# Performance work log

Measured on AMD Instinct MI355X. Metric: run time of the kernel, lower is better.

Reference implementation:

```python
import jax, jax.numpy as jnp
import numpy as np

NUM_CQ = 16
NUM_CODES = 8192
NUM_SAMPLES = 16
TEMP = 1.0
NHEADS = 4
DM = 32
EMB = 768
B, L = 64, 512


def setup_inputs():
    key = jax.random.key(0)
    ks = jax.random.split(key, 16)

    def lin(k, shape):
        fan_in = shape[-1]
        return (jax.random.uniform(k, shape, jnp.float32, -1.0, 1.0) / np.sqrt(fan_in)).astype(jnp.float32)

    xcq = jax.random.normal(ks[0], (B, L, EMB), jnp.float32)
    attn_mask = jax.random.randint(ks[1], (B, L - NUM_CQ), 0, 2, dtype=jnp.int32)
    cb = jax.random.normal(ks[2], (NUM_CODES, EMB), jnp.float32)
    codebook = 100.0 * cb / jnp.linalg.norm(cb, axis=-1, keepdims=True)  # matches 100*normalize init
    return dict(
        xcq=xcq, attn_mask=attn_mask,
        fc_in_w=lin(ks[3], (DM, EMB)), fc_in_b=jnp.zeros((DM,), jnp.float32),
        fc_out_w=lin(ks[4], (EMB, DM)), fc_out_b=jnp.zeros((EMB,), jnp.float32),
        enc_in_w=lin(ks[5], (2, 3 * DM, DM)), enc_in_b=jnp.zeros((2, 3 * DM), jnp.float32),
        enc_out_w=lin(ks[6], (2, DM, DM)), enc_out_b=jnp.zeros((2, DM), jnp.float32),
        enc_ff1_w=lin(ks[7], (2, 2 * DM, DM)), enc_ff1_b=jnp.zeros((2, 2 * DM), jnp.float32),
        enc_ff2_w=lin(ks[8], (2, DM, 2 * DM)), enc_ff2_b=jnp.zeros((2, DM), jnp.float32),
        enc_ln1_g=jnp.ones((2, DM), jnp.float32), enc_ln1_b=jnp.zeros((2, DM), jnp.float32),
        enc_ln2_g=jnp.ones((2, DM), jnp.float32), enc_ln2_b=jnp.zeros((2, DM), jnp.float32),
        codebook=codebook,
    )


def _layernorm(x, g, b):
    mu = jnp.mean(x, -1, keepdims=True)
    var = jnp.mean((x - mu) ** 2, -1, keepdims=True)
    return g * (x - mu) / jnp.sqrt(var + 1e-5) + b


def _forward(xcq, attn_mask, fc_in_w, fc_in_b, fc_out_w, fc_out_b,
             enc_in_w, enc_in_b, enc_out_w, enc_out_b,
             enc_ff1_w, enc_ff1_b, enc_ff2_w, enc_ff2_b,
             enc_ln1_g, enc_ln1_b, enc_ln2_g, enc_ln2_b, codebook):
    Bb, Ll, _ = xcq.shape
    dh = DM // NHEADS
    x = xcq @ fc_in_w.T + fc_in_b  # [B, L, 32]
    # ones for the cq tokens, then the provided mask; True = valid key
    valid = jnp.concatenate([jnp.ones((Bb, NUM_CQ), bool), attn_mask.astype(bool)], axis=1)  # [B, L]
    for l in range(2):  # torch post-norm TransformerEncoderLayer, relu, dropout=0 (eval)
        qkv = x @ enc_in_w[l].T + enc_in_b[l]
        q, k, v = jnp.split(qkv, 3, axis=-1)
        sh = lambda t: t.reshape(Bb, Ll, NHEADS, dh).transpose(0, 2, 1, 3)  # [B,h,L,dh]
        q, k, v = sh(q), sh(k), sh(v)
        scores = jnp.einsum('bhqd,bhkd->bhqk', q, k) / np.sqrt(dh)
        scores = jnp.where(valid[:, None, None, :], scores, -1e9)  # key padding mask
        attn = jax.nn.softmax(scores, axis=-1)
        o = jnp.einsum('bhqk,bhkd->bhqd', attn, v).transpose(0, 2, 1, 3).reshape(Bb, Ll, DM)
        o = o @ enc_out_w[l].T + enc_out_b[l]
        x = _layernorm(x + o, enc_ln1_g[l], enc_ln1_b[l])
        h = jax.nn.relu(x @ enc_ff1_w[l].T + enc_ff1_b[l]) @ enc_ff2_w[l].T + enc_ff2_b[l]
        x = _layernorm(x + h, enc_ln2_g[l], enc_ln2_b[l])
    xc_out = x[:, :NUM_CQ] @ fc_out_w.T + fc_out_b  # [B, ncq, 768]
    flat = xc_out.reshape(-1, EMB)  # [N, 768]
    dists = (jnp.sum(flat ** 2, 1, keepdims=True) + jnp.sum(codebook ** 2, 1)
             - 2.0 * (flat @ codebook.T))  # [N, K] squared euclidean
    logits = (-dists - 1e-5) / TEMP
    N = Bb * NUM_CQ
    # multinomial(total_count=NUM_SAMPLES): draw S categoricals per row and count
    draws = jax.random.categorical(jax.random.key(42), logits, shape=(NUM_SAMPLES, N))  # [S, N]
    rows = jnp.broadcast_to(jnp.arange(N), (NUM_SAMPLES, N))
    samples = jnp.zeros((N, NUM_CODES), jnp.float32).at[rows, draws].add(1.0)  # [N, K] counts
    xq = (samples @ codebook).reshape(xc_out.shape) / NUM_SAMPLES
    xc_quantized = xc_out + jax.lax.stop_gradient(xq - xc_out)  # straight-through estimator
    return xc_quantized


def reference(xcq, attn_mask, fc_in_w, fc_in_b, fc_out_w, fc_out_b,
              enc_in_w, enc_in_b, enc_out_w, enc_out_b,
              enc_ff1_w, enc_ff1_b, enc_ff2_w, enc_ff2_b,
              enc_ln1_g, enc_ln1_b, enc_ln2_g, enc_ln2_b, codebook):
    xc_quantized = _forward(xcq, attn_mask, fc_in_w, fc_in_b, fc_out_w, fc_out_b,
                            enc_in_w, enc_in_b, enc_out_w, enc_out_b,
                            enc_ff1_w, enc_ff1_b, enc_ff2_w, enc_ff2_b,
                            enc_ln1_g, enc_ln1_b, enc_ln2_g, enc_ln2_b, codebook)
    return (xc_quantized, xcq)
```

## Files before the change

kernel.cpp:

```cpp
#include <hip/hip_runtime.h>
#include <stdint.h>

#define NCODES 8192
#define NROWS 1024

#define OFF_LOGITS 0ll
#define OFF_X      8388608ll
#define OFF_QKV    9437184ll
#define OFF_ATTN   12582912ll
#define OFF_FLAT   13631488ll
#define OFF_CSQ    14418944ll

__device__ __forceinline__ uint32_t rotl32(uint32_t x, int r) { return (x << r) | (x >> (32 - r)); }

__device__ __forceinline__ void tf2x32_key42(uint32_t x0, uint32_t x1, uint32_t& o0, uint32_t& o1) {
  const uint32_t k0 = 0u, k1 = 42u;
  const uint32_t k2 = k0 ^ k1 ^ 0x1BD11BDAu;
  x0 += k0; x1 += k1;
  x0 += x1; x1 = rotl32(x1,13); x1 ^= x0;
  x0 += x1; x1 = rotl32(x1,15); x1 ^= x0;
  x0 += x1; x1 = rotl32(x1,26); x1 ^= x0;
  x0 += x1; x1 = rotl32(x1, 6); x1 ^= x0;
  x0 += k1; x1 += k2 + 1u;
  x0 += x1; x1 = rotl32(x1,17); x1 ^= x0;
  x0 += x1; x1 = rotl32(x1,29); x1 ^= x0;
  x0 += x1; x1 = rotl32(x1,16); x1 ^= x0;
  x0 += x1; x1 = rotl32(x1,24); x1 ^= x0;
  x0 += k2; x1 += k0 + 2u;
  x0 += x1; x1 = rotl32(x1,13); x1 ^= x0;
  x0 += x1; x1 = rotl32(x1,15); x1 ^= x0;
  x0 += x1; x1 = rotl32(x1,26); x1 ^= x0;
  x0 += x1; x1 = rotl32(x1, 6); x1 ^= x0;
  x0 += k0; x1 += k1 + 3u;
  x0 += x1; x1 = rotl32(x1,17); x1 ^= x0;
  x0 += x1; x1 = rotl32(x1,29); x1 ^= x0;
  x0 += x1; x1 = rotl32(x1,16); x1 ^= x0;
  x0 += x1; x1 = rotl32(x1,24); x1 ^= x0;
  x0 += k1; x1 += k2 + 4u;
  x0 += x1; x1 = rotl32(x1,13); x1 ^= x0;
  x0 += x1; x1 = rotl32(x1,15); x1 ^= x0;
  x0 += x1; x1 = rotl32(x1,26); x1 ^= x0;
  x0 += x1; x1 = rotl32(x1, 6); x1 ^= x0;
  x0 += k2; x1 += k0 + 5u;
  o0 = x0; o1 = x1;
}

__device__ __forceinline__ float gumbel_at(uint32_t idx) {
  uint32_t y0, y1;
  tf2x32_key42(0u, idx, y0, y1);
  uint32_t bits = y0 ^ y1;
  float f = __uint_as_float((bits >> 9) | 0x3f800000u) - 1.0f;
  float u = fmaxf(f, 1.17549435e-38f);
  return -logf(-logf(u));
}

__global__ __launch_bounds__(256) void k_fcin(const float* __restrict__ xcq,
                                              const float* __restrict__ W,
                                              const float* __restrict__ b,
                                              float* __restrict__ x,
                                              float* __restrict__ outcopy) {
  __shared__ float xs[64 * 36];
  int t = threadIdx.x;
  int w = t >> 6, lane = t & 63;
  long tb = (long)blockIdx.x * 64;
  const float4* xcq4 = (const float4*)xcq;
  float4* out4 = (float4*)outcopy;
  const float4* W4 = (const float4*)W;
  float acc[8];
  #pragma unroll
  for (int i = 0; i < 8; i++) acc[i] = 0.f;

  for (int jc4 = 0; jc4 < 192; jc4 += 8) {
    __syncthreads();
    #pragma unroll
    for (int p = 0; p < 2; p++) {
      int f = t + 256 * p;
      int row = f >> 3, j4 = f & 7;
      long g = (tb + row) * 192 + jc4 + j4;
      float4 v = xcq4[g];
      *(float4*)(xs + row * 36 + j4 * 4) = v;
      out4[g] = v;
    }
    __syncthreads();
    #pragma unroll
    for (int j4 = 0; j4 < 8; j4++) {
      float4 xv = *(const float4*)(xs + lane * 36 + j4 * 4);
      #pragma unroll
      for (int ci = 0; ci < 8; ci++) {
        int c = w * 8 + ci;
        float4 wv = W4[c * 192 + jc4 + j4];
        acc[ci] += xv.x * wv.x + xv.y * wv.y + xv.z * wv.z + xv.w * wv.w;
      }
    }
  }
  __syncthreads();
  *(float4*)(xs + lane * 36 + w * 8)     = make_float4(acc[0] + b[w*8+0], acc[1] + b[w*8+1], acc[2] + b[w*8+2], acc[3] + b[w*8+3]);
  *(float4*)(xs + lane * 36 + w * 8 + 4) = make_float4(acc[4] + b[w*8+4], acc[5] + b[w*8+5], acc[6] + b[w*8+6], acc[7] + b[w*8+7]);
  __syncthreads();
  float4* x4 = (float4*)x;
  #pragma unroll
  for (int p = 0; p < 2; p++) {
    int f = t + 256 * p;
    int row = f >> 3, c4 = f & 7;
    x4[(tb + row) * 8 + c4] = *(const float4*)(xs + row * 36 + c4 * 4);
  }
}

__global__ __launch_bounds__(64) void k_qkv(const float* __restrict__ x,
                                            const float* __restrict__ W,
                                            const float* __restrict__ b,
                                            float* __restrict__ qkv) {
  long token = (long)blockIdx.x * 64 + threadIdx.x;
  const float4* x4 = (const float4*)x;
  const float4* W4 = (const float4*)W;
  float4* q4 = (float4*)qkv;
  float4 xr[8];
  #pragma unroll
  for (int j4 = 0; j4 < 8; j4++) xr[j4] = x4[token * 8 + j4];
  #pragma unroll
  for (int c4 = 0; c4 < 24; c4++) {
    float s[4];
    #pragma unroll
    for (int q = 0; q < 4; q++) {
      int c = c4 * 4 + q;
      float acc = 0.f;
      #pragma unroll
      for (int j4 = 0; j4 < 8; j4++) {
        float4 wv = W4[c * 8 + j4];
        acc += xr[j4].x * wv.x + xr[j4].y * wv.y + xr[j4].z * wv.z + xr[j4].w * wv.w;
      }
      s[q] = acc + b[c];
    }
    q4[token * 24 + c4] = make_float4(s[0], s[1], s[2], s[3]);
  }
}

__global__ __launch_bounds__(256) void k_attn(const float* __restrict__ qkv,
                                              const int* __restrict__ amask,
                                              float* __restrict__ attno) {
  int z = blockIdx.x;
  int b = z >> 3;
  int h = (z >> 1) & 3;
  int half = z & 1;
  __shared__ float4 ks4[512 * 2];
  __shared__ float4 vs4[512 * 2];
  __shared__ float inval[512];
  int t = threadIdx.x;
  long qb4 = (long)b * 512 * 24;
  const float4* qkv4 = (const float4*)qkv;
  #pragma unroll
  for (int p = 0; p < 4; p++) {
    int f = t + 256 * p;
    int tok = f >> 1, hf = f & 1;
    ks4[f] = qkv4[qb4 + (long)tok * 24 + 8 + h * 2 + hf];
    vs4[f] = qkv4[qb4 + (long)tok * 24 + 16 + h * 2 + hf];
  }
  #pragma unroll
  for (int p = 0; p < 2; p++) {
    int l = t + 256 * p;
    inval[l] = (l < 16 || amask[b * 496 + (l - 16)] != 0) ? 0.f : 1.f;
  }
  __syncthreads();
  const float scale = 0.35355339059327373f;
  int lq = half * 256 + t;
  float4 qa = qkv4[qb4 + (long)lq * 24 + h * 2];
  float4 qb = qkv4[qb4 + (long)lq * 24 + h * 2 + 1];
  float m = -3.4e38f;
  for (int lk = 0; lk < 512; lk++) {
    float4 ka = ks4[lk * 2], kb = ks4[lk * 2 + 1];
    float s = qa.x*ka.x + qa.y*ka.y + qa.z*ka.z + qa.w*ka.w
            + qb.x*kb.x + qb.y*kb.y + qb.z*kb.z + qb.w*kb.w;
    s *= scale;
    s = inval[lk] != 0.f ? -1e9f : s;
    m = fmaxf(m, s);
  }
  float denom = 0.f;
  float4 o0 = make_float4(0,0,0,0), o1 = make_float4(0,0,0,0);
  for (int lk = 0; lk < 512; lk++) {
    float4 ka = ks4[lk * 2], kb = ks4[lk * 2 + 1];
    float s = qa.x*ka.x + qa.y*ka.y + qa.z*ka.z + qa.w*ka.w
            + qb.x*kb.x + qb.y*kb.y + qb.z*kb.z + qb.w*kb.w;
    s *= scale;
    s = inval[lk] != 0.f ? -1e9f : s;
    float p = expf(s - m);
    denom += p;
    float4 va = vs4[lk * 2], vb = vs4[lk * 2 + 1];
    o0.x += p * va.x; o0.y += p * va.y; o0.z += p * va.z; o0.w += p * va.w;
    o1.x += p * vb.x; o1.y += p * vb.y; o1.z += p * vb.z; o1.w += p * vb.w;
  }
  float inv = 1.f / denom;
  float4* a4 = (float4*)attno;
  long ob = ((long)b * 512 + lq) * 8 + h * 2;
  a4[ob]     = make_float4(o0.x*inv, o0.y*inv, o0.z*inv, o0.w*inv);
  a4[ob + 1] = make_float4(o1.x*inv, o1.y*inv, o1.z*inv, o1.w*inv);
}

__global__ __launch_bounds__(64) void k_oproj_ln(const float* __restrict__ attno,
                                                 const float* __restrict__ W,
                                                 const float* __restrict__ b,
                                                 const float* __restrict__ g,
                                                 const float* __restrict__ beta,
                                                 float* __restrict__ x) {
  long token = (long)blockIdx.x * 64 + threadIdx.x;
  const float4* a4 = (const float4*)attno;
  const float4* x4 = (const float4*)x;
  const float4* W4 = (const float4*)W;
  float4 orow[8];
  float xr[32];
  #pragma unroll
  for (int j4 = 0; j4 < 8; j4++) {
    orow[j4] = a4[token * 8 + j4];
    float4 v = x4[token * 8 + j4];
    xr[j4*4] = v.x; xr[j4*4+1] = v.y; xr[j4*4+2] = v.z; xr[j4*4+3] = v.w;
  }
  float v[32];
  #pragma unroll
  for (int c = 0; c < 32; c++) {
    float acc = 0.f;
    #pragma unroll
    for (int j4 = 0; j4 < 8; j4++) {
      float4 wv = W4[c * 8 + j4];
      acc += orow[j4].x * wv.x + orow[j4].y * wv.y + orow[j4].z * wv.z + orow[j4].w * wv.w;
    }
    v[c] = acc + b[c] + xr[c];
  }
  float mu = 0.f;
  #pragma unroll
  for (int c = 0; c < 32; c++) mu += v[c];
  mu *= 0.03125f;
  float var = 0.f;
  #pragma unroll
  for (int c = 0; c < 32; c++) { float d = v[c] - mu; var += d * d; }
  var *= 0.03125f;
  float inv = 1.f / sqrtf(var + 1e-5f);
  float4* xo4 = (float4*)x;
  #pragma unroll
  for (int j4 = 0; j4 < 8; j4++) {
    float4 o;
    o.x = g[j4*4]   * (v[j4*4]   - mu) * inv + beta[j4*4];
    o.y = g[j4*4+1] * (v[j4*4+1] - mu) * inv + beta[j4*4+1];
    o.z = g[j4*4+2] * (v[j4*4+2] - mu) * inv + beta[j4*4+2];
    o.w = g[j4*4+3] * (v[j4*4+3] - mu) * inv + beta[j4*4+3];
    xo4[token * 8 + j4] = o;
  }
}

__global__ __launch_bounds__(64) void k_ffn_ln(const float* __restrict__ x,
                                               const float* __restrict__ W1,
                                               const float* __restrict__ b1,
                                               const float* __restrict__ W2,
                                               const float* __restrict__ b2,
                                               const float* __restrict__ g,
                                               const float* __restrict__ beta,
                                               float* __restrict__ xout) {
  long token = (long)blockIdx.x * 64 + threadIdx.x;
  const float4* x4 = (const float4*)x;
  const float4* W14 = (const float4*)W1;
  const float4* W24 = (const float4*)W2;
  float xr[32];
  #pragma unroll
  for (int j4 = 0; j4 < 8; j4++) {
    float4 v = x4[token * 8 + j4];
    xr[j4*4] = v.x; xr[j4*4+1] = v.y; xr[j4*4+2] = v.z; xr[j4*4+3] = v.w;
  }
  float h[64];
  #pragma unroll
  for (int c = 0; c < 64; c++) {
    float acc = 0.f;
    #pragma unroll
    for (int j4 = 0; j4 < 8; j4++) {
      float4 wv = W14[c * 8 + j4];
      acc += xr[j4*4] * wv.x + xr[j4*4+1] * wv.y + xr[j4*4+2] * wv.z + xr[j4*4+3] * wv.w;
    }
    h[c] = fmaxf(acc + b1[c], 0.f);
  }
  float v[32];
  #pragma unroll
  for (int c = 0; c < 32; c++) {
    float acc = 0.f;
    #pragma unroll
    for (int j4 = 0; j4 < 16; j4++) {
      float4 wv = W24[c * 16 + j4];
      acc += h[j4*4] * wv.x + h[j4*4+1] * wv.y + h[j4*4+2] * wv.z + h[j4*4+3] * wv.w;
    }
    v[c] = acc + b2[c] + xr[c];
  }
  float mu = 0.f;
  #pragma unroll
  for (int c = 0; c < 32; c++) mu += v[c];
  mu *= 0.03125f;
  float var = 0.f;
  #pragma unroll
  for (int c = 0; c < 32; c++) { float d = v[c] - mu; var += d * d; }
  var *= 0.03125f;
  float inv = 1.f / sqrtf(var + 1e-5f);
  float4* xo4 = (float4*)xout;
  #pragma unroll
  for (int j4 = 0; j4 < 8; j4++) {
    float4 o;
    o.x = g[j4*4]   * (v[j4*4]   - mu) * inv + beta[j4*4];
    o.y = g[j4*4+1] * (v[j4*4+1] - mu) * inv + beta[j4*4+1];
    o.z = g[j4*4+2] * (v[j4*4+2] - mu) * inv + beta[j4*4+2];
    o.w = g[j4*4+3] * (v[j4*4+3] - mu) * inv + beta[j4*4+3];
    xo4[token * 8 + j4] = o;
  }
}

__global__ __launch_bounds__(256) void k_fcout(const float* __restrict__ x,
                                               const float* __restrict__ W,
                                               const float* __restrict__ b,
                                               float* __restrict__ flat) {
  int bb = blockIdx.x;
  __shared__ float xs[16 * 32];
  int t = threadIdx.x;
  if (t < 128) {
    int row = t >> 3, j4 = t & 7;
    *(float4*)(xs + row * 32 + j4 * 4) =
        *(const float4*)(x + ((long)bb * 512 + row) * 32 + j4 * 4);
  }
  __syncthreads();
  #pragma unroll
  for (int i = 0; i < 3; i++) {
    int e = t + 256 * i;
    const float4* w4 = (const float4*)(W + e * 32);
    float4 wv[8];
    #pragma unroll
    for (int j4 = 0; j4 < 8; j4++) wv[j4] = w4[j4];
    float bias = b[e];
    #pragma unroll
    for (int r = 0; r < 16; r++) {
      float s = 0.f;
      #pragma unroll
      for (int j4 = 0; j4 < 8; j4++) {
        const float* xr = xs + r * 32 + j4 * 4;
        s += xr[0] * wv[j4].x + xr[1] * wv[j4].y + xr[2] * wv[j4].z + xr[3] * wv[j4].w;
      }
      flat[((long)bb * 16 + r) * 768 + e] = s + bias;
    }
  }
}

__global__ __launch_bounds__(256) void k_cbsq(const float* __restrict__ cb,
                                              float* __restrict__ cb_sq) {
  int w = threadIdx.x >> 6, lane = threadIdx.x & 63;
  int k = blockIdx.x * 4 + w;
  const float* row = cb + (long)k * 768;
  float s = 0.f;
  #pragma unroll
  for (int i = 0; i < 12; i++) { float v = row[lane + 64 * i]; s += v * v; }
  #pragma unroll
  for (int off = 32; off >= 1; off >>= 1) s += __shfl_xor(s, off);
  if (lane == 0) cb_sq[k] = s;
}

__global__ __launch_bounds__(256, 2) void k_logits(const float* __restrict__ flat,
                                                   const float* __restrict__ cb,
                                                   const float* __restrict__ cb_sq,
                                                   float* __restrict__ logits) {
  int rb = blockIdx.x >> 5;
  int cblk = blockIdx.x & 31;
  __shared__ float fs[64 * 36];
  __shared__ float cs[256 * 36];
  int t = threadIdx.x;
  int r0 = (t >> 5) * 8;
  int c0 = t & 31;
  long frow = (long)rb * 64;
  long cbase = (long)cblk * 256;
  float acc[8][8];
  #pragma unroll
  for (int ri = 0; ri < 8; ri++)
    #pragma unroll
    for (int ci = 0; ci < 8; ci++) acc[ri][ci] = 0.f;

  for (int kc = 0; kc < 768; kc += 32) {
    __syncthreads();
    #pragma unroll
    for (int p = 0; p < 2; p++) {
      int f = t + 256 * p;
      int row = f >> 3, k4 = f & 7;
      *(float4*)(fs + row * 36 + k4 * 4) =
          *(const float4*)(flat + (frow + row) * 768 + kc + k4 * 4);
    }
    #pragma unroll
    for (int p = 0; p < 8; p++) {
      int col = p * 32 + (t >> 3), k4 = t & 7;
      *(float4*)(cs + col * 36 + k4 * 4) =
          *(const float4*)(cb + (cbase + col) * 768 + kc + k4 * 4);
    }
    __syncthreads();
    #pragma unroll
    for (int k4 = 0; k4 < 8; k4++) {
      float4 fa[8], fb[8];
      #pragma unroll
      for (int i = 0; i < 8; i++) fa[i] = *(const float4*)(fs + (r0 + i) * 36 + k4 * 4);
      #pragma unroll
      for (int i = 0; i < 8; i++) fb[i] = *(const float4*)(cs + (c0 + 32 * i) * 36 + k4 * 4);
      #pragma unroll
      for (int ri = 0; ri < 8; ri++) {
        #pragma unroll
        for (int ci = 0; ci < 8; ci++) {
          acc[ri][ci] = fmaf(fa[ri].x, fb[ci].x, acc[ri][ci]);
          acc[ri][ci] = fmaf(fa[ri].y, fb[ci].y, acc[ri][ci]);
          acc[ri][ci] = fmaf(fa[ri].z, fb[ci].z, acc[ri][ci]);
          acc[ri][ci] = fmaf(fa[ri].w, fb[ci].w, acc[ri][ci]);
        }
      }
    }
  }
  #pragma unroll
  for (int ci = 0; ci < 8; ci++) {
    long col = cbase + c0 + 32 * ci;
    float csq = cb_sq[col];
    #pragma unroll
    for (int ri = 0; ri < 8; ri++) {
      long n = frow + r0 + ri;
      logits[n * 8192 + col] = 2.f * acc[ri][ci] - csq - 1e-5f;
    }
  }
}

__global__ __launch_bounds__(256) void k_sample(const float* __restrict__ logits,
                                                const float* __restrict__ cb,
                                                const float* __restrict__ flat,
                                                float* __restrict__ out0) {
  int n = blockIdx.x, t = threadIdx.x;
  const float* lrow = logits + (long)n * 8192;
  __shared__ float s_max[4];
  __shared__ int s_cnt;
  __shared__ int cand[8192];
  __shared__ float redv[64];
  __shared__ int redi[64];
  __shared__ int draws[16];
  float m = -3.4e38f;
  for (int i = 0; i < 32; i++) m = fmaxf(m, lrow[t + 256 * i]);
  #pragma unroll
  for (int off = 32; off >= 1; off >>= 1) m = fmaxf(m, __shfl_xor(m, off));
  if ((t & 63) == 0) s_max[t >> 6] = m;
  if (t == 0) s_cnt = 0;
  __syncthreads();
  float rowmax = fmaxf(fmaxf(s_max[0], s_max[1]), fmaxf(s_max[2], s_max[3]));
  float thresh = rowmax - 20.5f;
  for (int i = 0; i < 32; i++) {
    int k = t + 256 * i;
    if (lrow[k] >= thresh) { int p = atomicAdd(&s_cnt, 1); cand[p] = k; }
  }
  __syncthreads();
  int ncand = s_cnt;
  float bv[16]; int bi[16];
  #pragma unroll
  for (int s = 0; s < 16; s++) { bv[s] = -3.4e38f; bi[s] = 0x7fffffff; }
  for (int c = t; c < ncand; c += 256) {
    int k = cand[c];
    float lg = lrow[k];
    #pragma unroll
    for (int s = 0; s < 16; s++) {
      uint32_t idx = ((uint32_t)((s << 10) + n) << 13) | (uint32_t)k;
      float val = gumbel_at(idx) + lg;
      if (val > bv[s] || (val == bv[s] && k < bi[s])) { bv[s] = val; bi[s] = k; }
    }
  }
  #pragma unroll
  for (int s = 0; s < 16; s++) {
    #pragma unroll
    for (int off = 32; off >= 1; off >>= 1) {
      float ov = __shfl_xor(bv[s], off);
      int oi = __shfl_xor(bi[s], off);
      if (ov > bv[s] || (ov == bv[s] && oi < bi[s])) { bv[s] = ov; bi[s] = oi; }
    }
    if ((t & 63) == 0) { redv[s * 4 + (t >> 6)] = bv[s]; redi[s * 4 + (t >> 6)] = bi[s]; }
  }
  __syncthreads();
  if (t < 16) {
    float bvv = redv[t * 4]; int bii = redi[t * 4];
    #pragma unroll
    for (int w = 1; w < 4; w++) {
      float ov = redv[t * 4 + w]; int oi = redi[t * 4 + w];
      if (ov > bvv || (ov == bvv && oi < bii)) { bvv = ov; bii = oi; }
    }
    draws[t] = bii;
  }
  __syncthreads();
  #pragma unroll
  for (int i = 0; i < 3; i++) {
    int e = t + 256 * i;
    float ssum = 0.f;
    #pragma unroll
    for (int s = 0; s < 16; s++) ssum += cb[(long)draws[s] * 768 + e];
    float xq = ssum * 0.0625f;
    float fl = flat[(long)n * 768 + e];
    out0[(long)n * 768 + e] = fl + (xq - fl);
  }
}

extern "C" void kernel_launch(void* const* d_in, const int* in_sizes, int n_in,
                              void* d_out, int out_size, void* d_ws, size_t ws_size,
                              hipStream_t stream) {
  (void)in_sizes; (void)n_in; (void)out_size; (void)ws_size;
  const float* xcq      = (const float*)d_in[0];
  const int*   amask    = (const int*)d_in[1];
  const float* fc_in_w  = (const float*)d_in[2];
  const float* fc_in_b  = (const float*)d_in[3];
  const float* fc_out_w = (const float*)d_in[4];
  const float* fc_out_b = (const float*)d_in[5];
  const float* enc_in_w = (const float*)d_in[6];
  const float* enc_in_b = (const float*)d_in[7];
  const float* enc_out_w= (const float*)d_in[8];
  const float* enc_out_b= (const float*)d_in[9];
  const float* ff1w     = (const float*)d_in[10];
  const float* ff1b     = (const float*)d_in[11];
  const float* ff2w     = (const float*)d_in[12];
  const float* ff2b     = (const float*)d_in[13];
  const float* ln1g     = (const float*)d_in[14];
  const float* ln1b     = (const float*)d_in[15];
  const float* ln2g     = (const float*)d_in[16];
  const float* ln2b     = (const float*)d_in[17];
  const float* cb       = (const float*)d_in[18];
  float* out = (float*)d_out;
  float* ws  = (float*)d_ws;

  float* x      = ws + OFF_X;
  float* qkv    = ws + OFF_QKV;
  float* attno  = ws + OFF_ATTN;
  float* flat   = ws + OFF_FLAT;
  float* csq    = ws + OFF_CSQ;
  float* logits = ws + OFF_LOGITS;

  k_fcin<<<512, 256, 0, stream>>>(xcq, fc_in_w, fc_in_b, x, out + 786432);
  for (int l = 0; l < 2; l++) {
    k_qkv<<<512, 64, 0, stream>>>(x, enc_in_w + l * 96 * 32, enc_in_b + l * 96, qkv);
    k_attn<<<512, 256, 0, stream>>>(qkv, amask, attno);
    k_oproj_ln<<<512, 64, 0, stream>>>(attno, enc_out_w + l * 32 * 32, enc_out_b + l * 32,
                                       ln1g + l * 32, ln1b + l * 32, x);
    k_ffn_ln<<<512, 64, 0, stream>>>(x, ff1w + l * 64 * 32, ff1b + l * 64,
                                     ff2w + l * 32 * 64, ff2b + l * 32,
                                     ln2g + l * 32, ln2b + l * 32, x);
  }
  k_fcout<<<64, 256, 0, stream>>>(x, fc_out_w, fc_out_b, flat);
  k_cbsq<<<2048, 256, 0, stream>>>(cb, csq);
  k_logits<<<512, 256, 0, stream>>>(flat, cb, csq, logits);
  k_sample<<<1024, 256, 0, stream>>>(logits, cb, flat, out);
}
```

Baseline: 1.108 ms.

## Compute approximate logits with bf16 MFMA and rescore candidates exactly in fp32

Replaces the fp32 SIMT logits GEMM with a bf16 MFMA GEMM on 128x128 tiles, with swizzled LDS so reads avoid bank conflicts. It first converts the codebook and the features to bf16 in separate kernels. Because bf16 scores are approximate, the sampler keeps a wider candidate window (rowmax-30 instead of -20.5) and recomputes exact fp32 dot products for those candidates before the Gumbel argmax. This trades the large fp32 GEMM for cheap matrix-core math, but adds conversion passes and per-candidate 768-length dot products, and relies on the widened threshold to preserve exact sampling.

```diff
diff --git a/kernel.cpp b/kernel.cpp
--- a/kernel.cpp
+++ b/kernel.cpp
@@ -353,96 +353,126 @@
   if (lane == 0) cb_sq[k] = s;
 }
 
-__global__ __launch_bounds__(256, 2) void k_logits(const float* __restrict__ flat,
-                                                   const float* __restrict__ cb,
-                                                   const float* __restrict__ cb_sq,
-                                                   float* __restrict__ logits) {
-  int rb = blockIdx.x >> 5;
-  int cblk = blockIdx.x & 31;
-  __shared__ float fs[64 * 36];
-  __shared__ float cs[256 * 36];
+__device__ __forceinline__ ushort f2bf(float x) {
+  uint32_t u = __float_as_uint(x);
+  uint32_t r = (u + 0x7fffu + ((u >> 16) & 1u)) >> 16;
+  return (ushort)r;
+}
+
+__global__ __launch_bounds__(256) void k_tobf16(const float* __restrict__ src,
+                                                ushort* __restrict__ dst, long n4) {
+  long i = (long)blockIdx.x * 256 + threadIdx.x;
+  if (i >= n4) return;
+  float4 v = ((const float4*)src)[i];
+  ushort4 o;
+  o.x = f2bf(v.x); o.y = f2bf(v.y); o.z = f2bf(v.z); o.w = f2bf(v.w);
+  ((ushort4*)dst)[i] = o;
+}
+
+typedef __attribute__((ext_vector_type(8))) short bf16x8;
+typedef __attribute__((ext_vector_type(4))) float f32x4;
+
+__global__ __launch_bounds__(256, 2) void k_logits_mfma(const ushort* __restrict__ fbf,
+                                                        const ushort* __restrict__ cbbf,
+                                                        float* __restrict__ approx) {
+  __shared__ __align__(16) short As[128 * 64];
+  __shared__ __align__(16) short Bs[128 * 64];
   int t = threadIdx.x;
-  int r0 = (t >> 5) * 8;
-  int c0 = t & 31;
-  long frow = (long)rb * 64;
-  long cbase = (long)cblk * 256;
-  float acc[8][8];
-  #pragma unroll
-  for (int ri = 0; ri < 8; ri++)
-    #pragma unroll
-    for (int ci = 0; ci < 8; ci++) acc[ri][ci] = 0.f;
-
-  for (int kc = 0; kc < 768; kc += 32) {
+  int mb = blockIdx.x & 7;
+  int nb = blockIdx.x >> 3;
+  int w = t >> 6, lane = t & 63;
+  int wr = w >> 1, wc = w & 1;
+
+  f32x4 zero; zero.x = 0.f; zero.y = 0.f; zero.z = 0.f; zero.w = 0.f;
+  f32x4 acc[4][4];
+  #pragma unroll
+  for (int i = 0; i < 4; i++)
+    #pragma unroll
+    for (int j = 0; j < 4; j++) acc[i][j] = zero;
+
+  for (int kt = 0; kt < 12; kt++) {
+    int kc = kt * 64;
+    bf16x8 ra[4], rb[4];
+    #pragma unroll
+    for (int p = 0; p < 4; p++) {
+      int li = p * 256 + t;
+      int row = li >> 3, s = li & 7;
+      ra[p] = *(const bf16x8*)(fbf + (long)(mb * 128 + row) * 768 + kc + s * 8);
+      rb[p] = *(const bf16x8*)(cbbf + (long)(nb * 128 + row) * 768 + kc + s * 8);
+    }
     __syncthreads();
     #pragma unroll
-    for (int p = 0; p < 2; p++) {
-      int f = t + 256 * p;
-      int row = f >> 3, k4 = f & 7;
-      *(float4*)(fs + row * 36 + k4 * 4) =
-          *(const float4*)(flat + (frow + row) * 768 + kc + k4 * 4);
-    }
-    #pragma unroll
-    for (int p = 0; p < 8; p++) {
-      int col = p * 32 + (t >> 3), k4 = t & 7;
-      *(float4*)(cs + col * 36 + k4 * 4) =
-          *(const float4*)(cb + (cbase + col) * 768 + kc + k4 * 4);
+    for (int p = 0; p < 4; p++) {
+      int li = p * 256 + t;
+      int row = li >> 3, s = li & 7, ss = s ^ (row & 7);
+      *(bf16x8*)(As + row * 64 + ss * 8) = ra[p];
+      *(bf16x8*)(Bs + row * 64 + ss * 8) = rb[p];
     }
     __syncthreads();
     #pragma unroll
-    for (int k4 = 0; k4 < 8; k4++) {
-      float4 fa[8], fb[8];
+    for (int ks = 0; ks < 2; ks++) {
+      int slot = ks * 4 + (lane >> 4);
+      bf16x8 a[4], b[4];
       #pragma unroll
-      for (int i = 0; i < 8; i++) fa[i] = *(const float4*)(fs + (r0 + i) * 36 + k4 * 4);
+      for (int i = 0; i < 4; i++) {
+        int rowa = wr * 64 + i * 16 + (lane & 15);
+        a[i] = *(const bf16x8*)(As + rowa * 64 + (slot ^ (rowa & 7)) * 8);
+        int rowb = wc * 64 + i * 16 + (lane & 15);
+        b[i] = *(const bf16x8*)(Bs + rowb * 64 + (slot ^ (rowb & 7)) * 8);
+      }
       #pragma unroll
-      for (int i = 0; i < 8; i++) fb[i] = *(const float4*)(cs + (c0 + 32 * i) * 36 + k4 * 4);
-      #pragma unroll
-      for (int ri = 0; ri < 8; ri++) {
+      for (int i = 0; i < 4; i++)
         #pragma unroll
-        for (int ci = 0; ci < 8; ci++) {
-          acc[ri][ci] = fmaf(fa[ri].x, fb[ci].x, acc[ri][ci]);
-          acc[ri][ci] = fmaf(fa[ri].y, fb[ci].y, acc[ri][ci]);
-          acc[ri][ci] = fmaf(fa[ri].z, fb[ci].z, acc[ri][ci]);
-          acc[ri][ci] = fmaf(fa[ri].w, fb[ci].w, acc[ri][ci]);
-        }
-      }
-    }
-  }
-  #pragma unroll
-  for (int ci = 0; ci < 8; ci++) {
-    long col = cbase + c0 + 32 * ci;
-    float csq = cb_sq[col];
-    #pragma unroll
-    for (int ri = 0; ri < 8; ri++) {
-      long n = frow + r0 + ri;
-      logits[n * 8192 + col] = 2.f * acc[ri][ci] - csq - 1e-5f;
-    }
-  }
-}
-
-__global__ __launch_bounds__(256) void k_sample(const float* __restrict__ logits,
+        for (int j = 0; j < 4; j++)
+          acc[i][j] = __builtin_amdgcn_mfma_f32_16x16x32_bf16(a[i], b[j], acc[i][j], 0, 0, 0);
+    }
+  }
+  long rbase = (long)mb * 128 + wr * 64 + (lane >> 4) * 4;
+  int cbase = nb * 128 + wc * 64 + (lane & 15);
+  #pragma unroll
+  for (int i = 0; i < 4; i++) {
+    #pragma unroll
+    for (int j = 0; j < 4; j++) {
+      f32x4 v = acc[i][j];
+      long r0 = rbase + i * 16;
+      int c = cbase + j * 16;
+      approx[(r0 + 0) * 8192 + c] = 2.f * v.x;
+      approx[(r0 + 1) * 8192 + c] = 2.f * v.y;
+      approx[(r0 + 2) * 8192 + c] = 2.f * v.z;
+      approx[(r0 + 3) * 8192 + c] = 2.f * v.w;
+    }
+  }
+}
+
+__global__ __launch_bounds__(256) void k_sample(const float* __restrict__ approx,
                                                 const float* __restrict__ cb,
+                                                const float* __restrict__ csq,
                                                 const float* __restrict__ flat,
                                                 float* __restrict__ out0) {
   int n = blockIdx.x, t = threadIdx.x;
-  const float* lrow = logits + (long)n * 8192;
+  const float* arow = approx + (long)n * 8192;
   __shared__ float s_max[4];
   __shared__ int s_cnt;
   __shared__ int cand[8192];
+  __shared__ float fs[768];
   __shared__ float redv[64];
   __shared__ int redi[64];
   __shared__ int draws[16];
+  if (t < 192) ((float4*)fs)[t] = ((const float4*)(flat + (long)n * 768))[t];
+  float va[32];
   float m = -3.4e38f;
-  for (int i = 0; i < 32; i++) m = fmaxf(m, lrow[t + 256 * i]);
+  #pragma unroll
+  for (int i = 0; i < 32; i++) { va[i] = arow[t + 256 * i]; m = fmaxf(m, va[i]); }
   #pragma unroll
   for (int off = 32; off >= 1; off >>= 1) m = fmaxf(m, __shfl_xor(m, off));
   if ((t & 63) == 0) s_max[t >> 6] = m;
   if (t == 0) s_cnt = 0;
   __syncthreads();
   float rowmax = fmaxf(fmaxf(s_max[0], s_max[1]), fmaxf(s_max[2], s_max[3]));
-  float thresh = rowmax - 20.5f;
+  float thresh = rowmax - 30.0f;
+  #pragma unroll
   for (int i = 0; i < 32; i++) {
-    int k = t + 256 * i;
-    if (lrow[k] >= thresh) { int p = atomicAdd(&s_cnt, 1); cand[p] = k; }
+    if (va[i] >= thresh) { int p = atomicAdd(&s_cnt, 1); cand[p] = t + 256 * i; }
   }
   __syncthreads();
   int ncand = s_cnt;
@@ -451,7 +481,18 @@
   for (int s = 0; s < 16; s++) { bv[s] = -3.4e38f; bi[s] = 0x7fffffff; }
   for (int c = t; c < ncand; c += 256) {
     int k = cand[c];
-    float lg = lrow[k];
+    const float4* cb4 = (const float4*)(cb + (long)k * 768);
+    float acc = 0.f;
+    #pragma unroll 8
+    for (int j4 = 0; j4 < 192; j4++) {
+      float4 wv = cb4[j4];
+      const float* xr = fs + j4 * 4;
+      acc = fmaf(xr[0], wv.x, acc);
+      acc = fmaf(xr[1], wv.y, acc);
+      acc = fmaf(xr[2], wv.z, acc);
+      acc = fmaf(xr[3], wv.w, acc);
+    }
+    float lg = 2.f * acc - csq[k] - 1e-5f;
     #pragma unroll
     for (int s = 0; s < 16; s++) {
       uint32_t idx = ((uint32_t)((s << 10) + n) << 13) | (uint32_t)k;
@@ -487,7 +528,7 @@
     #pragma unroll
     for (int s = 0; s < 16; s++) ssum += cb[(long)draws[s] * 768 + e];
     float xq = ssum * 0.0625f;
-    float fl = flat[(long)n * 768 + e];
+    float fl = fs[e];
     out0[(long)n * 768 + e] = fl + (xq - fl);
   }
 }
@@ -523,7 +564,9 @@
   float* attno  = ws + OFF_ATTN;
   float* flat   = ws + OFF_FLAT;
   float* csq    = ws + OFF_CSQ;
-  float* logits = ws + OFF_LOGITS;
+  float* approx = ws + OFF_LOGITS;
+  ushort* cbbf  = (ushort*)(ws + OFF_QKV);
+  ushort* fbf   = (ushort*)(ws + OFF_ATTN);
 
   k_fcin<<<512, 256, 0, stream>>>(xcq, fc_in_w, fc_in_b, x, out + 786432);
   for (int l = 0; l < 2; l++) {
@@ -537,6 +580,8 @@
   }
   k_fcout<<<64, 256, 0, stream>>>(x, fc_out_w, fc_out_b, flat);
   k_cbsq<<<2048, 256, 0, stream>>>(cb, csq);
-  k_logits<<<512, 256, 0, stream>>>(flat, cb, csq, logits);
-  k_sample<<<1024, 256, 0, stream>>>(logits, cb, flat, out);
-}
+  k_tobf16<<<6144, 256, 0, stream>>>(cb, cbbf, 1572864ll);
+  k_tobf16<<<768, 256, 0, stream>>>(flat, fbf, 196608ll);
+  k_logits_mfma<<<512, 256, 0, stream>>>(fbf, cbbf, approx);
+  k_sample<<<1024, 256, 0, stream>>>(approx, cb, csq, flat, out);
+}
```

After: 984.4 us. 11.1% less time.
